# Kernel optimization log

Measured on AMD Instinct MI355X. Metric: run time of the kernel, lower is better.

The kernel has to match this reference:

```python
import jax, jax.numpy as jnp
import numpy as np

PAGE_SIZE = 64  # page size of the 64-token page table (get_page_table_64)


def setup_inputs() -> dict:
    key = jax.random.key(0)
    k1, k2, k3, k4 = jax.random.split(key, 4)
    b, h, d = 64, 64, 128
    num_blocks = 128
    num_pages = b * num_blocks
    query = jax.random.normal(k1, (b, h, d), dtype=jnp.float32)
    weights = jax.random.normal(k2, (b, h), dtype=jnp.float32)
    index_k_cache = jax.random.normal(k3, (num_pages, PAGE_SIZE, d), dtype=jnp.float32)
    # each batch row gets its own distinct pages (all indices in range)
    block_tables = jnp.arange(b * num_blocks, dtype=jnp.int32).reshape(b, num_blocks)
    seq_lens = jax.random.randint(k4, (b,), 1, num_blocks * PAGE_SIZE, dtype=jnp.int32)
    return {
        "query": query,
        "weights": weights,
        "index_k_cache": index_k_cache,
        "block_tables": block_tables,
        "seq_lens": seq_lens,
    }


def reference(query, weights, index_k_cache, block_tables, seq_lens):
    # Faithful translation of triton_mqa_logits_kernel (paged MQA ReLU-weighted
    # QK logits for the top-k indexer).
    b, h, d = query.shape
    num_blocks = block_tables.shape[1]
    max_seq_len = num_blocks * PAGE_SIZE
    # Gather paged KV per block table: [b, num_blocks, PAGE, d] -> [b, S, d]
    k = index_k_cache[block_tables].reshape(b, max_seq_len, d)
    # s[b,h,s] = q . k  (MQA: single K shared across index heads)
    s = jnp.einsum("bhd,bsd->bhs", query, k)
    # ReLU then per-head weighted sum over heads -> [b, S]
    logits = jnp.einsum("bh,bhs->bs", weights, jax.nn.relu(s))
    # positions beyond the sequence length are invalid (-inf, as in the ragged
    # path all_qk_logits init, so downstream top-k never selects them)
    pos = jnp.arange(max_seq_len, dtype=jnp.int32)
    mask = pos[None, :] < seq_lens[:, None]
    return jnp.where(mask, logits, -jnp.inf).astype(jnp.float32)
```

## Files before the change

kernel.cpp:

```cpp
#include <hip/hip_runtime.h>
#include <hip/hip_bf16.h>

#define B 64
#define H 64
#define D 128
#define NB 128
#define PAGE 64
#define SMAX (NB * PAGE)
#define TILE_S 128
#define NEG_BIG (-3.0e38f)

typedef __attribute__((ext_vector_type(8))) short bf16x8;
typedef __attribute__((ext_vector_type(4))) float f32x4;

__device__ __forceinline__ unsigned int rnd16(float f) {
    union { float f; unsigned int u; } v; v.f = f;
    return v.u + 0x8000u;
}
__device__ __forceinline__ unsigned int pack2(float lo, float hi) {
    return __builtin_amdgcn_perm(rnd16(hi), rnd16(lo), 0x07060302);
}
__device__ __forceinline__ bf16x8 cvt8(float4 a, float4 b) {
    union { unsigned int u[4]; bf16x8 v; } r;
    r.u[0] = pack2(a.x, a.y); r.u[1] = pack2(a.z, a.w);
    r.u[2] = pack2(b.x, b.y); r.u[3] = pack2(b.z, b.w);
    return r.v;
}

__device__ __forceinline__ void load_lds16(const void* g, void* l) {
    __builtin_amdgcn_global_load_lds(
        (const __attribute__((address_space(1))) unsigned int*)g,
        (__attribute__((address_space(3))) unsigned int*)l,
        16, 0, 0);
}

__global__ __launch_bounds__(256) void q_prep(
    const float* __restrict__ query, unsigned int* __restrict__ qws)
{
    const int b = blockIdx.x, tid = threadIdx.x;
    const float* qb = query + (size_t)b * H * D;
    unsigned int* ob = qws + (size_t)b * 4096;
    #pragma unroll
    for (int i = 0; i < 4; ++i) {
        const int idx = i * 256 + tid;
        const int h = idx >> 4, c = idx & 15;
        const float4 f0 = *(const float4*)(qb + h * D + c * 8);
        const float4 f1 = *(const float4*)(qb + h * D + c * 8 + 4);
        uint4 o;
        o.x = pack2(f0.x, f0.y); o.y = pack2(f0.z, f0.w);
        o.z = pack2(f1.x, f1.y); o.w = pack2(f1.z, f1.w);
        const int slot = h * 16 + (c ^ (h & 15));
        *(uint4*)(ob + slot * 4) = o;
    }
}

__global__ __launch_bounds__(256) void indexer_kernel(
    const unsigned int* __restrict__ qws,
    const float* __restrict__ weights,
    const float* __restrict__ kcache,
    const int*   __restrict__ block_tables,
    const int*   __restrict__ seq_lens,
    float*       __restrict__ out)
{
    const int b    = blockIdx.y;
    const int tile = blockIdx.x;
    const int tid  = threadIdx.x;
    const int slen = seq_lens[b];

    if (tile * TILE_S >= slen) {
        if (tid < TILE_S)
            out[(size_t)b * SMAX + tile * TILE_S + tid] = NEG_BIG;
        return;
    }

    __shared__ __align__(16) unsigned short q_lds[H * 16 * 8];

    const int wv = tid >> 6, ln = tid & 63;
    const int quad = ln >> 4, lm = ln & 15;

    {
        const unsigned int* src = qws + (size_t)b * 4096 + wv * 1024;
        #pragma unroll
        for (int j = 0; j < 4; ++j)
            load_lds16(src + j * 256 + ln * 4,
                       &q_lds[(wv * 1024 + j * 256) * 2]);
    }

    const int wbase = tile * TILE_S + wv * 32;
    const bool wactive = wbase < slen;

    float4 kf[2][4][2];
    if (wactive) {
        #pragma unroll
        for (int mi = 0; mi < 2; ++mi) {
            const int pos  = wbase + mi * 16 + lm;
            const int page = block_tables[b * NB + (pos >> 6)];
            const float* rowp = kcache + ((size_t)page * PAGE + (pos & 63)) * D;
            #pragma unroll
            for (int kc = 0; kc < 4; ++kc) {
                kf[mi][kc][0] = *(const float4*)(rowp + kc * 32 + quad * 8);
                kf[mi][kc][1] = *(const float4*)(rowp + kc * 32 + quad * 8 + 4);
            }
        }
    }

    __syncthreads();

    if (!wactive) {
        if (ln < 32) out[(size_t)b * SMAX + wbase + ln] = NEG_BIG;
        return;
    }

    f32x4 acc[2][4] = {};
    #pragma unroll
    for (int kc = 0; kc < 4; ++kc) {
        bf16x8 a[2];
        #pragma unroll
        for (int mi = 0; mi < 2; ++mi)
            a[mi] = cvt8(kf[mi][kc][0], kf[mi][kc][1]);
        bf16x8 q[4];
        #pragma unroll
        for (int ni = 0; ni < 4; ++ni) {
            const int h = ni * 16 + lm;
            const int slot = h * 16 + ((kc * 4 + quad) ^ lm);
            q[ni] = *(const bf16x8*)&q_lds[slot * 8];
        }
        #pragma unroll
        for (int mi = 0; mi < 2; ++mi)
            #pragma unroll
            for (int ni = 0; ni < 4; ++ni)
                acc[mi][ni] = __builtin_amdgcn_mfma_f32_16x16x32_bf16(
                    a[mi], q[ni], acc[mi][ni], 0, 0, 0);
    }

    float w[4];
    #pragma unroll
    for (int ni = 0; ni < 4; ++ni)
        w[ni] = weights[b * H + ni * 16 + lm];

    #pragma unroll
    for (int mi = 0; mi < 2; ++mi) {
        #pragma unroll
        for (int r = 0; r < 4; ++r) {
            float v = 0.f;
            #pragma unroll
            for (int ni = 0; ni < 4; ++ni)
                v = fmaf(w[ni], fmaxf(acc[mi][ni][r], 0.f), v);
            v += __shfl_xor(v, 1);
            v += __shfl_xor(v, 2);
            v += __shfl_xor(v, 4);
            v += __shfl_xor(v, 8);
            if (lm == 0) {
                const int pos = wbase + mi * 16 + quad * 4 + r;
                out[(size_t)b * SMAX + pos] = (pos < slen) ? v : NEG_BIG;
            }
        }
    }
}

extern "C" void kernel_launch(void* const* d_in, const int* in_sizes, int n_in,
                              void* d_out, int out_size, void* d_ws, size_t ws_size,
                              hipStream_t stream) {
    const float* query   = (const float*)d_in[0];
    const float* weights = (const float*)d_in[1];
    const float* kcache  = (const float*)d_in[2];
    const int*   bt      = (const int*)d_in[3];
    const int*   sl      = (const int*)d_in[4];
    float*       out     = (float*)d_out;
    unsigned int* qws    = (unsigned int*)d_ws;

    q_prep<<<B, 256, 0, stream>>>(query, qws);
    dim3 grid(SMAX / TILE_S, B);
    indexer_kernel<<<grid, 256, 0, stream>>>(qws, weights, kcache, bt, sl, out);
}
```

Baseline: 337.6 us.

## Stage one K page per block into swizzled LDS via async global-to-LDS loads

The indexer kernel now handles one 64-token page per block. The whole fp32 page is copied into LDS with global_load_lds, using an XOR swizzle so the later reads avoid bank conflicts, instead of each lane loading K rows into registers. The tile shrinks from 128 to 64 tokens, which doubles the grid, cuts accumulators per wave, and removes the per-row block-table lookup. q_prep is also split across 4x more blocks. The cost is 32KB of LDS per block, which may limit occupancy, and each block now does less work.

```diff
diff --git a/kernel.cpp b/kernel.cpp
--- a/kernel.cpp
+++ b/kernel.cpp
@@ -7,7 +7,7 @@
 #define NB 128
 #define PAGE 64
 #define SMAX (NB * PAGE)
-#define TILE_S 128
+#define TILE_S 64
 #define NEG_BIG (-3.0e38f)
 
 typedef __attribute__((ext_vector_type(8))) short bf16x8;
@@ -37,21 +37,17 @@
 __global__ __launch_bounds__(256) void q_prep(
     const float* __restrict__ query, unsigned int* __restrict__ qws)
 {
-    const int b = blockIdx.x, tid = threadIdx.x;
+    const int b = blockIdx.x >> 2, i = blockIdx.x & 3, tid = threadIdx.x;
     const float* qb = query + (size_t)b * H * D;
     unsigned int* ob = qws + (size_t)b * 4096;
-    #pragma unroll
-    for (int i = 0; i < 4; ++i) {
-        const int idx = i * 256 + tid;
-        const int h = idx >> 4, c = idx & 15;
-        const float4 f0 = *(const float4*)(qb + h * D + c * 8);
-        const float4 f1 = *(const float4*)(qb + h * D + c * 8 + 4);
-        uint4 o;
-        o.x = pack2(f0.x, f0.y); o.y = pack2(f0.z, f0.w);
-        o.z = pack2(f1.x, f1.y); o.w = pack2(f1.z, f1.w);
-        const int slot = h * 16 + (c ^ (h & 15));
-        *(uint4*)(ob + slot * 4) = o;
-    }
+    const int idx = i * 256 + tid;
+    const int h = idx >> 4, c = idx & 15;
+    const float4 f0 = *(const float4*)(qb + h * D + c * 8);
+    const float4 f1 = *(const float4*)(qb + h * D + c * 8 + 4);
+    uint4 o;
+    o.x = pack2(f0.x, f0.y); o.y = pack2(f0.z, f0.w);
+    o.z = pack2(f1.x, f1.y); o.w = pack2(f1.z, f1.w);
+    *(uint4*)(ob + (h * 16 + (c ^ (h & 15))) * 4) = o;
 }
 
 __global__ __launch_bounds__(256) void indexer_kernel(
@@ -73,11 +69,22 @@
         return;
     }
 
+    __shared__ __align__(16) float k_lds[TILE_S * D];
     __shared__ __align__(16) unsigned short q_lds[H * 16 * 8];
 
     const int wv = tid >> 6, ln = tid & 63;
     const int quad = ln >> 4, lm = ln & 15;
 
+    const int page = block_tables[b * NB + tile];
+    const float* pbase = kcache + (size_t)page * PAGE * D;
+
+    #pragma unroll
+    for (int j = 0; j < 8; ++j) {
+        const int r  = wv * 16 + j * 2 + (ln >> 5);
+        const int cs = ln & 31;
+        const int cg = cs ^ (r & 15);
+        load_lds16(pbase + r * D + cg * 4, &k_lds[(wv * 16 + j * 2) * D]);
+    }
     {
         const unsigned int* src = qws + (size_t)b * 4096 + wv * 1024;
         #pragma unroll
@@ -85,52 +92,28 @@
             load_lds16(src + j * 256 + ln * 4,
                        &q_lds[(wv * 1024 + j * 256) * 2]);
     }
-
-    const int wbase = tile * TILE_S + wv * 32;
-    const bool wactive = wbase < slen;
-
-    float4 kf[2][4][2];
-    if (wactive) {
-        #pragma unroll
-        for (int mi = 0; mi < 2; ++mi) {
-            const int pos  = wbase + mi * 16 + lm;
-            const int page = block_tables[b * NB + (pos >> 6)];
-            const float* rowp = kcache + ((size_t)page * PAGE + (pos & 63)) * D;
-            #pragma unroll
-            for (int kc = 0; kc < 4; ++kc) {
-                kf[mi][kc][0] = *(const float4*)(rowp + kc * 32 + quad * 8);
-                kf[mi][kc][1] = *(const float4*)(rowp + kc * 32 + quad * 8 + 4);
-            }
-        }
-    }
-
     __syncthreads();
 
-    if (!wactive) {
-        if (ln < 32) out[(size_t)b * SMAX + wbase + ln] = NEG_BIG;
+    const int wbase = tile * TILE_S + wv * 16;
+    if (wbase >= slen) {
+        if (ln < 16) out[(size_t)b * SMAX + wbase + ln] = NEG_BIG;
         return;
     }
 
-    f32x4 acc[2][4] = {};
+    f32x4 acc[4] = {};
     #pragma unroll
     for (int kc = 0; kc < 4; ++kc) {
-        bf16x8 a[2];
-        #pragma unroll
-        for (int mi = 0; mi < 2; ++mi)
-            a[mi] = cvt8(kf[mi][kc][0], kf[mi][kc][1]);
-        bf16x8 q[4];
+        const int row = wv * 16 + lm;
+        const int c0  = kc * 8 + quad * 2;
+        const float4 f0 = *(const float4*)&k_lds[row * D + ((c0    ) ^ lm) * 4];
+        const float4 f1 = *(const float4*)&k_lds[row * D + ((c0 + 1) ^ lm) * 4];
+        const bf16x8 a = cvt8(f0, f1);
         #pragma unroll
         for (int ni = 0; ni < 4; ++ni) {
-            const int h = ni * 16 + lm;
-            const int slot = h * 16 + ((kc * 4 + quad) ^ lm);
-            q[ni] = *(const bf16x8*)&q_lds[slot * 8];
+            const int slot = (ni * 16 + lm) * 16 + ((kc * 4 + quad) ^ lm);
+            const bf16x8 q = *(const bf16x8*)&q_lds[slot * 8];
+            acc[ni] = __builtin_amdgcn_mfma_f32_16x16x32_bf16(a, q, acc[ni], 0, 0, 0);
         }
-        #pragma unroll
-        for (int mi = 0; mi < 2; ++mi)
-            #pragma unroll
-            for (int ni = 0; ni < 4; ++ni)
-                acc[mi][ni] = __builtin_amdgcn_mfma_f32_16x16x32_bf16(
-                    a[mi], q[ni], acc[mi][ni], 0, 0, 0);
     }
 
     float w[4];
@@ -139,21 +122,18 @@
         w[ni] = weights[b * H + ni * 16 + lm];
 
     #pragma unroll
-    for (int mi = 0; mi < 2; ++mi) {
+    for (int r = 0; r < 4; ++r) {
+        float v = 0.f;
         #pragma unroll
-        for (int r = 0; r < 4; ++r) {
-            float v = 0.f;
-            #pragma unroll
-            for (int ni = 0; ni < 4; ++ni)
-                v = fmaf(w[ni], fmaxf(acc[mi][ni][r], 0.f), v);
-            v += __shfl_xor(v, 1);
-            v += __shfl_xor(v, 2);
-            v += __shfl_xor(v, 4);
-            v += __shfl_xor(v, 8);
-            if (lm == 0) {
-                const int pos = wbase + mi * 16 + quad * 4 + r;
-                out[(size_t)b * SMAX + pos] = (pos < slen) ? v : NEG_BIG;
-            }
+        for (int ni = 0; ni < 4; ++ni)
+            v = fmaf(w[ni], fmaxf(acc[ni][r], 0.f), v);
+        v += __shfl_xor(v, 1);
+        v += __shfl_xor(v, 2);
+        v += __shfl_xor(v, 4);
+        v += __shfl_xor(v, 8);
+        if (lm == 0) {
+            const int pos = wbase + quad * 4 + r;
+            out[(size_t)b * SMAX + pos] = (pos < slen) ? v : NEG_BIG;
         }
     }
 }
@@ -169,7 +149,7 @@
     float*       out     = (float*)d_out;
     unsigned int* qws    = (unsigned int*)d_ws;
 
-    q_prep<<<B, 256, 0, stream>>>(query, qws);
+    q_prep<<<B * 4, 256, 0, stream>>>(query, qws);
     dim3 grid(SMAX / TILE_S, B);
     indexer_kernel<<<grid, 256, 0, stream>>>(qws, weights, kcache, bt, sl, out);
 }
```

Measured after the change: 333.2 us. About the same (-1.3%).
